# Performance work log

Measured on AMD Instinct MI355X. Metric: run time of the kernel, lower is better.

The kernel has to match this reference:

```python
import jax, jax.numpy as jnp
import numpy as np


def setup_inputs() -> dict:
    key = jax.random.key(0)
    ks = jax.random.split(key, 24)
    N, C, D_IN, HID, EMB = 8192, 4096, 32, 128, 128
    s = 0.05
    inp = {
        "cand_feat": jax.random.normal(ks[0], (1, C, D_IN), jnp.float32),
        "graph_pos": jax.random.uniform(ks[1], (N, 3), jnp.float32),
        "graph_rad": jax.random.uniform(ks[2], (N,), jnp.float32) + 0.01,
        "L": jnp.ones((1,), jnp.float32),
        "adj": jax.random.uniform(ks[3], (N, N), jnp.float32),
        "mask": jax.random.randint(ks[4], (1, C), 0, 2, jnp.int32),
        # candidate encoder: 32 -> 128 -> 128
        "cW1": jax.random.normal(ks[5], (D_IN, 128), jnp.float32) * s,
        "cb1": jnp.zeros((128,), jnp.float32),
        "cW2": jax.random.normal(ks[6], (128, EMB), jnp.float32) * s,
        "cb2": jnp.zeros((EMB,), jnp.float32),
        # graph encoder input proj: 4 -> 128
        "gW0": jax.random.normal(ks[7], (4, HID), jnp.float32) * s,
        "gb0": jnp.zeros((HID,), jnp.float32),
        # 3 GNN layers: concat(2*HID) -> HID
        "gnnW": jax.random.normal(ks[8], (3, 2 * HID, HID), jnp.float32) * s,
        "gnnb": jnp.zeros((3, HID), jnp.float32),
        # output proj: 2*HID -> EMB
        "goW": jax.random.normal(ks[9], (2 * HID, EMB), jnp.float32) * s,
        "gob": jnp.zeros((EMB,), jnp.float32),
        # fusion: 2*EMB -> 256 -> 128 -> 1
        "fW1": jax.random.normal(ks[10], (2 * EMB, 256), jnp.float32) * s,
        "fb1": jnp.zeros((256,), jnp.float32),
        "fW2": jax.random.normal(ks[11], (256, 128), jnp.float32) * s,
        "fb2": jnp.zeros((128,), jnp.float32),
        "fW3": jax.random.normal(ks[12], (128, 1), jnp.float32) * s,
        "fb3": jnp.zeros((1,), jnp.float32),
    }
    return inp


def reference(cand_feat, graph_pos, graph_rad, L, adj, mask,
              cW1, cb1, cW2, cb2, gW0, gb0, gnnW, gnnb, goW, gob,
              fW1, fb1, fW2, fb2, fW3, fb3):
    relu = jax.nn.relu
    # ---- candidate encoder: [1, C, 32] -> [1, C, 128]
    cand_emb = relu(relu(cand_feat @ cW1 + cb1) @ cW2 + cb2)
    # ---- graph encoder ----
    node = jnp.concatenate([graph_pos / L, (graph_rad / jnp.max(graph_rad))[:, None]], axis=1)  # [N, 4]
    h = relu(node @ gW0 + gb0)  # [N, HID]
    deg = jnp.clip(jnp.sum(adj, axis=-1, keepdims=True), 1.0)  # [N, 1]
    for i in range(gnnW.shape[0]):
        agg = (adj @ h) / deg                       # degree-normalized aggregation
        h = relu(jnp.concatenate([h, agg], axis=-1) @ gnnW[i] + gnnb[i])
    h_glob = jnp.concatenate([jnp.max(h, axis=0), jnp.mean(h, axis=0)], axis=-1)  # [2*HID]
    graph_emb = h_glob @ goW + gob  # [EMB]
    # ---- fusion decoder ----
    g_exp = jnp.broadcast_to(graph_emb[None, None, :], cand_emb.shape)
    combined = jnp.concatenate([cand_emb, g_exp], axis=-1)  # [1, C, 2*EMB]
    scores = (relu(relu(combined @ fW1 + fb1) @ fW2 + fb2) @ fW3 + fb3)[..., 0]  # [1, C]
    return jnp.where(mask == 0, -jnp.inf, scores)
```

## Files before the change

### kernel.cpp

```cpp
#include <hip/hip_runtime.h>
#include <hip/hip_bf16.h>

constexpr int NN  = 8192;
constexpr int CC  = 4096;
constexpr int HD  = 128;
constexpr int KSPLIT = 16;

typedef __attribute__((ext_vector_type(8))) short bf16x8;
typedef __attribute__((ext_vector_type(4))) short s16x4;
typedef __attribute__((ext_vector_type(4))) float f32x4;

static __device__ __forceinline__ unsigned short f2bf(float f) {
  unsigned int u = __builtin_bit_cast(unsigned int, f);
  unsigned int lsb = (u >> 16) & 1u;
  u += 0x7fffu + lsb;
  return (unsigned short)(u >> 16);
}
static __device__ __forceinline__ float bf2f(unsigned short u) {
  return __builtin_bit_cast(float, ((unsigned int)u) << 16);
}

static __device__ __forceinline__ int swz(int r, int k) {
  return r * 128 + ((((k >> 3) ^ (r & 7))) << 4) + ((k & 7) * 2);
}

#define GL16(gp, lp)                                                              \
  __builtin_amdgcn_global_load_lds(                                               \
      (const __attribute__((address_space(1))) void*)(gp),                        \
      (__attribute__((address_space(3))) void*)(lp), 16, 0, 0)

__global__ __launch_bounds__(256) void k_radmax(const float* __restrict__ rad, float* out) {
  __shared__ float red[256];
  int t = threadIdx.x;
  float m = 0.0f;
  for (int i = t; i < NN; i += 256) m = fmaxf(m, rad[i]);
  red[t] = m; __syncthreads();
  for (int s = 128; s > 0; s >>= 1) {
    if (t < s) red[t] = fmaxf(red[t], red[t + s]);
    __syncthreads();
  }
  if (t == 0) out[0] = red[0];
}

__global__ __launch_bounds__(256) void k_h0(const float* __restrict__ pos, const float* __restrict__ rad,
                                            const float* __restrict__ Lp, const float* __restrict__ rmax,
                                            const float* __restrict__ gW0, const float* __restrict__ gb0,
                                            float* __restrict__ h, unsigned short* __restrict__ hT) {
  __shared__ __align__(16) unsigned short lt[128][72];
  int t = threadIdx.x;
  int i0 = blockIdx.x * 64;
  float invL = 1.0f / Lp[0];
  float invR = 1.0f / rmax[0];
  for (int rep = 0; rep < 32; ++rep) {
    int idx = rep * 256 + t;
    int il = idx >> 7, j = idx & 127;
    int i = i0 + il;
    float n0 = pos[i * 3 + 0] * invL, n1 = pos[i * 3 + 1] * invL, n2 = pos[i * 3 + 2] * invL;
    float n3 = rad[i] * invR;
    float v = gb0[j] + n0 * gW0[j] + n1 * gW0[128 + j] + n2 * gW0[256 + j] + n3 * gW0[384 + j];
    v = fmaxf(v, 0.0f);
    h[(size_t)i * HD + j] = v;
    lt[j][il] = f2bf(v);
  }
  __syncthreads();
  int j = t >> 1, half = t & 1;
  unsigned short* dst = hT + (size_t)j * NN + i0 + half * 32;
  const uint4* src = (const uint4*)&lt[j][half * 32];
  uint4* d4 = (uint4*)dst;
  d4[0] = src[0]; d4[1] = src[1]; d4[2] = src[2]; d4[3] = src[3];
}

template <int SRC, int WRITEB, int DEG>
__global__ __launch_bounds__(256) void k_gemm(const float* __restrict__ A32,
                                              const unsigned short* __restrict__ A16,
                                              const unsigned short* __restrict__ hT,
                                              unsigned short* __restrict__ adjb,
                                              float* __restrict__ part_deg,
                                              unsigned short* __restrict__ part) {
  __shared__ uint4 AsQ[512];
  __shared__ uint4 BsQ[1024];
  char* As = (char*)AsQ;
  char* Bs = (char*)BsQ;
  const int t = threadIdx.x;
  const int bm = blockIdx.x;
  const int ks = blockIdx.y;
  const int kchunk = NN / KSPLIT;
  const int kbase = ks * kchunk;
  const int ksteps = kchunk / 64;

  const int lane = t & 63, w = t >> 6;
  const int wr = (w >> 1) * 32, wc = (w & 1) * 64;
  const int lr = lane & 15, lk4 = (lane >> 4) * 4;

  f32x4 acc[2][4];
  #pragma unroll
  for (int a = 0; a < 2; ++a)
    #pragma unroll
    for (int b = 0; b < 4; ++b) acc[a][b] = f32x4{0.f, 0.f, 0.f, 0.f};

  const int srow = t >> 3;
  const int sgl  = (t & 7) ^ (srow & 7);
  const unsigned short* bSrc[4];
  #pragma unroll
  for (int it = 0; it < 4; ++it)
    bSrc[it] = hT + (size_t)(it * 32 + srow) * NN + kbase + sgl * 8;

  const unsigned short* aSrc[2];
  if (SRC == 1) {
    #pragma unroll
    for (int it = 0; it < 2; ++it)
      aSrc[it] = A16 + (size_t)(bm * 64 + it * 32 + srow) * NN + kbase + sgl * 8;
  }
  const int ar = t >> 2, agq = (t & 3) * 2;
  const float* a32Src = nullptr;
  if (SRC == 0) a32Src = A32 + (size_t)(bm * 64 + ar) * NN + kbase + agq * 8;

  float rs = 0.f;

  for (int step = 0; step < ksteps; ++step) {
    __syncthreads();
    if (SRC == 1) {
      GL16(aSrc[0] + step * 64, As + t * 16);
      GL16(aSrc[1] + step * 64, As + 4096 + t * 16);
      #pragma unroll
      for (int it = 0; it < 4; ++it)
        GL16(bSrc[it] + step * 64, Bs + it * 4096 + t * 16);
    } else {
      const float* src = a32Src + step * 64;
      float4 v0 = ((const float4*)src)[0], v1 = ((const float4*)src)[1];
      float4 v2 = ((const float4*)src)[2], v3 = ((const float4*)src)[3];
      union { unsigned short u[16]; uint4 q[2]; } pk;
      pk.u[0]  = f2bf(v0.x); pk.u[1]  = f2bf(v0.y); pk.u[2]  = f2bf(v0.z); pk.u[3]  = f2bf(v0.w);
      pk.u[4]  = f2bf(v1.x); pk.u[5]  = f2bf(v1.y); pk.u[6]  = f2bf(v1.z); pk.u[7]  = f2bf(v1.w);
      pk.u[8]  = f2bf(v2.x); pk.u[9]  = f2bf(v2.y); pk.u[10] = f2bf(v2.z); pk.u[11] = f2bf(v2.w);
      pk.u[12] = f2bf(v3.x); pk.u[13] = f2bf(v3.y); pk.u[14] = f2bf(v3.z); pk.u[15] = f2bf(v3.w);
      if (DEG) rs += v0.x + v0.y + v0.z + v0.w + v1.x + v1.y + v1.z + v1.w
                   + v2.x + v2.y + v2.z + v2.w + v3.x + v3.y + v3.z + v3.w;
      if (WRITEB) {
        uint4* wdst = (uint4*)(adjb + (size_t)(bm * 64 + ar) * NN + kbase + step * 64 + agq * 8);
        wdst[0] = pk.q[0]; wdst[1] = pk.q[1];
      }
      *(uint4*)(As + ar * 128 + ((agq ^ (ar & 7)) << 4))       = pk.q[0];
      *(uint4*)(As + ar * 128 + (((agq + 1) ^ (ar & 7)) << 4)) = pk.q[1];
      #pragma unroll
      for (int it = 0; it < 4; ++it)
        GL16(bSrc[it] + step * 64, Bs + it * 4096 + t * 16);
    }
    __syncthreads();
    #pragma unroll
    for (int kk = 0; kk < 2; ++kk) {
      int klo = kk * 32 + lk4;
      bf16x8 a[2];
      #pragma unroll
      for (int mi = 0; mi < 2; ++mi) {
        int r = wr + mi * 16 + lr;
        union { bf16x8 v; s16x4 p[2]; } ua;
        ua.p[0] = *(const s16x4*)(As + swz(r, klo));
        ua.p[1] = *(const s16x4*)(As + swz(r, klo + 16));
        a[mi] = ua.v;
      }
      #pragma unroll
      for (int ni = 0; ni < 4; ++ni) {
        int rn = wc + ni * 16 + lr;
        union { bf16x8 v; s16x4 p[2]; } ub;
        ub.p[0] = *(const s16x4*)(Bs + swz(rn, klo));
        ub.p[1] = *(const s16x4*)(Bs + swz(rn, klo + 16));
        bf16x8 b = ub.v;
        #pragma unroll
        for (int mi = 0; mi < 2; ++mi)
          acc[mi][ni] = __builtin_amdgcn_mfma_f32_16x16x32_bf16(a[mi], b, acc[mi][ni], 0, 0, 0);
      }
    }
  }

  if (DEG) {
    float v = rs;
    v += __shfl_xor(v, 1);
    v += __shfl_xor(v, 2);
    if ((t & 3) == 0) part_deg[(size_t)ks * NN + bm * 64 + ar] = v;
  }

  unsigned short* outb = part + (size_t)ks * NN * HD;
  #pragma unroll
  for (int mi = 0; mi < 2; ++mi) {
    int rowb = bm * 64 + wr + mi * 16 + (lane >> 4) * 4;
    #pragma unroll
    for (int ni = 0; ni < 4; ++ni) {
      int col = wc + ni * 16 + lr;
      #pragma unroll
      for (int j = 0; j < 4; ++j)
        outb[(size_t)(rowb + j) * HD + col] = f2bf(acc[mi][ni][j]);
    }
  }
}

__global__ __launch_bounds__(256) void k_update(const unsigned short* __restrict__ part,
                                                const float* __restrict__ part_deg,
                                                const float* __restrict__ hin,
                                                const float* __restrict__ W, const float* __restrict__ bias,
                                                float* __restrict__ hout, unsigned short* __restrict__ hT,
                                                int last) {
  __shared__ float cc[16][256];
  __shared__ __align__(16) unsigned short lt2[128][24];
  int t = threadIdx.x;
  int r0 = blockIdx.x * 16;
  for (int rep = 0; rep < 8; ++rep) {
    int idx = rep * 256 + t;
    int rl = idx >> 7, j = idx & 127;
    int row = r0 + rl;
    float s = 0.f, d = 0.f;
    for (int ks = 0; ks < KSPLIT; ++ks) {
      s += bf2f(part[((size_t)ks * NN + row) * HD + j]);
      d += part_deg[(size_t)ks * NN + row];
    }
    d = fmaxf(d, 1.0f);
    cc[rl][128 + j] = s / d;
    cc[rl][j] = hin[(size_t)row * HD + j];
  }
  __syncthreads();
  int jo = t & 127, rbase = t >> 7;
  float accv[8];
  float bj = bias[jo];
  for (int rr = 0; rr < 8; ++rr) accv[rr] = bj;
  for (int jj = 0; jj < 256; ++jj) {
    float wv = W[jj * HD + jo];
    for (int rr = 0; rr < 8; ++rr) accv[rr] += cc[rbase + rr * 2][jj] * wv;
  }
  for (int rr = 0; rr < 8; ++rr) {
    int rl = rbase + rr * 2;
    float v = fmaxf(accv[rr], 0.f);
    hout[(size_t)(r0 + rl) * HD + jo] = v;
    if (!last) lt2[jo][rl] = f2bf(v);
  }
  if (!last) {
    __syncthreads();
    int j = t >> 1, half = t & 1;
    *(uint4*)(hT + (size_t)j * NN + r0 + half * 8) = *(const uint4*)&lt2[j][half * 8];
  }
}

__global__ __launch_bounds__(256) void k_pool(const float* __restrict__ h,
                                              float* __restrict__ pmax, float* __restrict__ psum) {
  int b = blockIdx.x, t = threadIdx.x;
  int j = t & 127, half = t >> 7;
  int r0 = b * 128 + half * 64;
  float mx = -1e30f, sm = 0.f;
  for (int r = r0; r < r0 + 64; ++r) {
    float v = h[(size_t)r * HD + j];
    mx = fmaxf(mx, v); sm += v;
  }
  __shared__ float lm[2][128], ls[2][128];
  lm[half][j] = mx; ls[half][j] = sm;
  __syncthreads();
  if (half == 0) {
    pmax[b * 128 + j] = fmaxf(lm[0][j], lm[1][j]);
    psum[b * 128 + j] = ls[0][j] + ls[1][j];
  }
}

__global__ __launch_bounds__(256) void k_glob(const float* __restrict__ pmax, const float* __restrict__ psum,
                                              const float* __restrict__ goW, const float* __restrict__ gob,
                                              float* __restrict__ ge) {
  __shared__ float hg[256];
  int t = threadIdx.x;
  int j = t & 127, which = t >> 7;
  if (which == 0) {
    float m = -1e30f;
    for (int b = 0; b < 64; ++b) m = fmaxf(m, pmax[b * 128 + j]);
    hg[j] = m;
  } else {
    float s = 0.f;
    for (int b = 0; b < 64; ++b) s += psum[b * 128 + j];
    hg[128 + j] = s * (1.0f / (float)NN);
  }
  __syncthreads();
  if (t < 128) {
    float s = gob[t];
    for (int jj = 0; jj < 256; ++jj) s += hg[jj] * goW[jj * HD + t];
    ge[t] = s;
  }
}

__global__ __launch_bounds__(256) void k_fusion(const float* __restrict__ cand, const float* __restrict__ ge,
                                                const int* __restrict__ mask,
                                                const float* __restrict__ cW1, const float* __restrict__ cb1,
                                                const float* __restrict__ cW2, const float* __restrict__ cb2,
                                                const float* __restrict__ fW1, const float* __restrict__ fb1,
                                                const float* __restrict__ fW2, const float* __restrict__ fb2,
                                                const float* __restrict__ fW3, const float* __restrict__ fb3,
                                                float* __restrict__ out) {
  __shared__ float x[16][32];
  __shared__ float t1[16][128];
  __shared__ float t2[16][128];
  __shared__ float u1[16][256];
  __shared__ float u2[16][129];
  __shared__ float geL[128];
  int t = threadIdx.x;
  int c0 = blockIdx.x * 16;
  if (t < 128) geL[t] = ge[t];
  for (int rep = 0; rep < 2; ++rep) {
    int idx = rep * 256 + t;
    int cl = idx >> 5, d = idx & 31;
    x[cl][d] = cand[(size_t)(c0 + cl) * 32 + d];
  }
  __syncthreads();
  {
    int j = t & 127, cg = (t >> 7) * 8;
    float a[8]; float bj = cb1[j];
    for (int q = 0; q < 8; ++q) a[q] = bj;
    for (int d = 0; d < 32; ++d) {
      float wv = cW1[d * 128 + j];
      for (int q = 0; q < 8; ++q) a[q] += x[cg + q][d] * wv;
    }
    for (int q = 0; q < 8; ++q) t1[cg + q][j] = fmaxf(a[q], 0.f);
  }
  __syncthreads();
  {
    int j = t & 127, cg = (t >> 7) * 8;
    float a[8]; float bj = cb2[j];
    for (int q = 0; q < 8; ++q) a[q] = bj;
    for (int d = 0; d < 128; ++d) {
      float wv = cW2[d * 128 + j];
      for (int q = 0; q < 8; ++q) a[q] += t1[cg + q][d] * wv;
    }
    for (int q = 0; q < 8; ++q) t2[cg + q][j] = fmaxf(a[q], 0.f);
  }
  __syncthreads();
  {
    int jo = t;
    float gp = fb1[jo];
    for (int d = 0; d < 128; ++d) gp += geL[d] * fW1[(128 + d) * 256 + jo];
    float a[16];
    for (int q = 0; q < 16; ++q) a[q] = gp;
    for (int d = 0; d < 128; ++d) {
      float wv = fW1[d * 256 + jo];
      for (int q = 0; q < 16; ++q) a[q] += t2[q][d] * wv;
    }
    for (int q = 0; q < 16; ++q) u1[q][jo] = fmaxf(a[q], 0.f);
  }
  __syncthreads();
  {
    int j = t & 127, cg = (t >> 7) * 8;
    float a[8]; float bj = fb2[j];
    for (int q = 0; q < 8; ++q) a[q] = bj;
    for (int d = 0; d < 256; ++d) {
      float wv = fW2[d * 128 + j];
      for (int q = 0; q < 8; ++q) a[q] += u1[cg + q][d] * wv;
    }
    for (int q = 0; q < 8; ++q) u2[cg + q][j] = fmaxf(a[q], 0.f);
  }
  __syncthreads();
  if (t < 16) {
    int c = c0 + t;
    float s = fb3[0];
    for (int d = 0; d < 128; ++d) s += u2[t][d] * fW3[d];
    out[c] = (mask[c] == 0) ? -3.0e38f : s;
  }
}

extern "C" void kernel_launch(void* const* d_in, const int* in_sizes, int n_in,
                              void* d_out, int out_size, void* d_ws, size_t ws_size,
                              hipStream_t stream) {
  const float* cand = (const float*)d_in[0];
  const float* pos  = (const float*)d_in[1];
  const float* rad  = (const float*)d_in[2];
  const float* Lp   = (const float*)d_in[3];
  const float* adj  = (const float*)d_in[4];
  const int*   mask = (const int*)d_in[5];
  const float* cW1 = (const float*)d_in[6];
  const float* cb1 = (const float*)d_in[7];
  const float* cW2 = (const float*)d_in[8];
  const float* cb2 = (const float*)d_in[9];
  const float* gW0 = (const float*)d_in[10];
  const float* gb0 = (const float*)d_in[11];
  const float* gnnW = (const float*)d_in[12];
  const float* gnnb = (const float*)d_in[13];
  const float* goW = (const float*)d_in[14];
  const float* gob = (const float*)d_in[15];
  const float* fW1 = (const float*)d_in[16];
  const float* fb1 = (const float*)d_in[17];
  const float* fW2 = (const float*)d_in[18];
  const float* fb2 = (const float*)d_in[19];
  const float* fW3 = (const float*)d_in[20];
  const float* fb3 = (const float*)d_in[21];

  char* ws = (char*)d_ws;
  float* h           = (float*)ws;
  unsigned short* hT = (unsigned short*)(ws + (4ull << 20));
  float* rmax        = (float*)(ws + (6ull << 20));
  float* pmax        = (float*)(ws + (6ull << 20) + 4096);
  float* psum        = pmax + 64 * 128;
  float* ge          = psum + 64 * 128;
  unsigned short* part = (unsigned short*)(ws + (8ull << 20));
  float* part_deg    = (float*)(ws + (40ull << 20));
  unsigned short* adjb = (unsigned short*)(ws + (41ull << 20));

  bool big = ws_size >= (41ull << 20) + (size_t)NN * NN * 2;

  k_radmax<<<1, 256, 0, stream>>>(rad, rmax);
  k_h0<<<NN / 64, 256, 0, stream>>>(pos, rad, Lp, rmax, gW0, gb0, h, hT);

  dim3 g(NN / 64, KSPLIT);
  for (int l = 0; l < 3; ++l) {
    if (l == 0) {
      if (big) k_gemm<0, 1, 1><<<g, 256, 0, stream>>>(adj, nullptr, hT, adjb, part_deg, part);
      else     k_gemm<0, 0, 1><<<g, 256, 0, stream>>>(adj, nullptr, hT, nullptr, part_deg, part);
    } else {
      if (big) k_gemm<1, 0, 0><<<g, 256, 0, stream>>>(nullptr, adjb, hT, nullptr, nullptr, part);
      else     k_gemm<0, 0, 0><<<g, 256, 0, stream>>>(adj, nullptr, hT, nullptr, nullptr, part);
    }
    k_update<<<NN / 16, 256, 0, stream>>>(part, part_deg, h,
                                          gnnW + l * 256 * HD, gnnb + l * HD, h, hT, l == 2);
  }
  k_pool<<<64, 256, 0, stream>>>(h, pmax, psum);
  k_glob<<<1, 256, 0, stream>>>(pmax, psum, goW, gob, ge);
  k_fusion<<<CC / 16, 256, 0, stream>>>(cand, ge, mask, cW1, cb1, cW2, cb2,
                                        fW1, fb1, fW2, fb2, fW3, fb3, (float*)d_out);
}
```

Measured before the change: 403.4 us.

## Split adj conversion into standalone kernel and double-buffer bf16 GEMM loads

```diff
diff --git a/kernel.cpp b/kernel.cpp
--- a/kernel.cpp
+++ b/kernel.cpp
@@ -4,7 +4,8 @@
 constexpr int NN  = 8192;
 constexpr int CC  = 4096;
 constexpr int HD  = 128;
-constexpr int KSPLIT = 16;
+constexpr int KSPLIT = 8;
+constexpr int KSTEPS = (NN / KSPLIT) / 64;
 
 typedef __attribute__((ext_vector_type(8))) short bf16x8;
 typedef __attribute__((ext_vector_type(4))) short s16x4;
@@ -70,23 +71,70 @@
   d4[0] = src[0]; d4[1] = src[1]; d4[2] = src[2]; d4[3] = src[3];
 }
 
-template <int SRC, int WRITEB, int DEG>
+template <int CONVERT>
+__global__ __launch_bounds__(256) void k_conv(const float* __restrict__ adj,
+                                              unsigned short* __restrict__ adjb,
+                                              float* __restrict__ deg) {
+  int row = blockIdx.x;
+  int t = threadIdx.x;
+  const float4* src = (const float4*)(adj + (size_t)row * NN);
+  float s = 0.f;
+  #pragma unroll
+  for (int it = 0; it < 4; ++it) {
+    int g = (it * 256 + t) * 2;
+    float4 v0 = src[g], v1 = src[g + 1];
+    s += v0.x + v0.y + v0.z + v0.w + v1.x + v1.y + v1.z + v1.w;
+    if (CONVERT) {
+      union { unsigned short u[8]; uint4 q; } pk;
+      pk.u[0] = f2bf(v0.x); pk.u[1] = f2bf(v0.y); pk.u[2] = f2bf(v0.z); pk.u[3] = f2bf(v0.w);
+      pk.u[4] = f2bf(v1.x); pk.u[5] = f2bf(v1.y); pk.u[6] = f2bf(v1.z); pk.u[7] = f2bf(v1.w);
+      *(uint4*)(adjb + (size_t)row * NN + (size_t)g * 4) = pk.q;
+    }
+  }
+  for (int o = 32; o > 0; o >>= 1) s += __shfl_down(s, o);
+  __shared__ float red[4];
+  if ((t & 63) == 0) red[t >> 6] = s;
+  __syncthreads();
+  if (t == 0) deg[row] = fmaxf(red[0] + red[1] + red[2] + red[3], 1.0f);
+}
+
+#define COMPUTE(Ab, Bb)                                                              \
+  _Pragma("unroll")                                                                  \
+  for (int kk = 0; kk < 2; ++kk) {                                                   \
+    int klo = kk * 32 + lk4;                                                         \
+    bf16x8 afr[2];                                                                   \
+    _Pragma("unroll")                                                                \
+    for (int mi = 0; mi < 2; ++mi) {                                                 \
+      int r = wr + mi * 16 + lr;                                                     \
+      union { bf16x8 v; s16x4 p[2]; } ua;                                            \
+      ua.p[0] = *(const s16x4*)((Ab) + swz(r, klo));                                 \
+      ua.p[1] = *(const s16x4*)((Ab) + swz(r, klo + 16));                            \
+      afr[mi] = ua.v;                                                                \
+    }                                                                                \
+    _Pragma("unroll")                                                                \
+    for (int ni = 0; ni < 4; ++ni) {                                                 \
+      int rn = wc + ni * 16 + lr;                                                    \
+      union { bf16x8 v; s16x4 p[2]; } ub;                                            \
+      ub.p[0] = *(const s16x4*)((Bb) + swz(rn, klo));                                \
+      ub.p[1] = *(const s16x4*)((Bb) + swz(rn, klo + 16));                           \
+      _Pragma("unroll")                                                              \
+      for (int mi = 0; mi < 2; ++mi)                                                 \
+        acc[mi][ni] = __builtin_amdgcn_mfma_f32_16x16x32_bf16(afr[mi], ub.v,         \
+                                                              acc[mi][ni], 0, 0, 0); \
+    }                                                                                \
+  }
+
+template <int SRC>
 __global__ __launch_bounds__(256) void k_gemm(const float* __restrict__ A32,
                                               const unsigned short* __restrict__ A16,
                                               const unsigned short* __restrict__ hT,
-                                              unsigned short* __restrict__ adjb,
-                                              float* __restrict__ part_deg,
                                               unsigned short* __restrict__ part) {
-  __shared__ uint4 AsQ[512];
-  __shared__ uint4 BsQ[1024];
-  char* As = (char*)AsQ;
-  char* Bs = (char*)BsQ;
+  __shared__ __align__(16) char As[2][8192];
+  __shared__ __align__(16) char Bs[2][16384];
   const int t = threadIdx.x;
   const int bm = blockIdx.x;
   const int ks = blockIdx.y;
-  const int kchunk = NN / KSPLIT;
-  const int kbase = ks * kchunk;
-  const int ksteps = kchunk / 64;
+  const int kbase = ks * (NN / KSPLIT);
 
   const int lane = t & 63, w = t >> 6;
   const int wr = (w >> 1) * 32, wc = (w & 1) * 64;
@@ -105,27 +153,43 @@
   for (int it = 0; it < 4; ++it)
     bSrc[it] = hT + (size_t)(it * 32 + srow) * NN + kbase + sgl * 8;
 
-  const unsigned short* aSrc[2];
   if (SRC == 1) {
+    const unsigned short* aSrc[2];
     #pragma unroll
     for (int it = 0; it < 2; ++it)
       aSrc[it] = A16 + (size_t)(bm * 64 + it * 32 + srow) * NN + kbase + sgl * 8;
-  }
-  const int ar = t >> 2, agq = (t & 3) * 2;
-  const float* a32Src = nullptr;
-  if (SRC == 0) a32Src = A32 + (size_t)(bm * 64 + ar) * NN + kbase + agq * 8;
-
-  float rs = 0.f;
-
-  for (int step = 0; step < ksteps; ++step) {
-    __syncthreads();
-    if (SRC == 1) {
-      GL16(aSrc[0] + step * 64, As + t * 16);
-      GL16(aSrc[1] + step * 64, As + 4096 + t * 16);
-      #pragma unroll
-      for (int it = 0; it < 4; ++it)
-        GL16(bSrc[it] + step * 64, Bs + it * 4096 + t * 16);
-    } else {
+
+#define STG(s, d) do {                                  \
+    GL16(aSrc[0] + (s) * 64, &As[d][t * 16]);           \
+    GL16(aSrc[1] + (s) * 64, &As[d][4096 + t * 16]);    \
+    GL16(bSrc[0] + (s) * 64, &Bs[d][t * 16]);           \
+    GL16(bSrc[1] + (s) * 64, &Bs[d][4096 + t * 16]);    \
+    GL16(bSrc[2] + (s) * 64, &Bs[d][8192 + t * 16]);    \
+    GL16(bSrc[3] + (s) * 64, &Bs[d][12288 + t * 16]);   \
+  } while (0)
+
+    STG(0, 0);
+    int cur = 0;
+    for (int step = 0; step < KSTEPS; ++step) {
+      if (step + 1 < KSTEPS) {
+        STG(step + 1, cur ^ 1);
+        asm volatile("s_waitcnt vmcnt(6)" ::: "memory");
+      } else {
+        asm volatile("s_waitcnt vmcnt(0)" ::: "memory");
+      }
+      __builtin_amdgcn_s_barrier();
+      __builtin_amdgcn_sched_barrier(0);
+      COMPUTE(As[cur], Bs[cur]);
+      __builtin_amdgcn_sched_barrier(0);
+      __builtin_amdgcn_s_barrier();
+      cur ^= 1;
+    }
+#undef STG
+  } else {
+    const int ar = t >> 2, agq = (t & 3) * 2;
+    const float* a32Src = A32 + (size_t)(bm * 64 + ar) * NN + kbase + agq * 8;
+    for (int step = 0; step < KSTEPS; ++step) {
+      __syncthreads();
       const float* src = a32Src + step * 64;
       float4 v0 = ((const float4*)src)[0], v1 = ((const float4*)src)[1];
       float4 v2 = ((const float4*)src)[2], v3 = ((const float4*)src)[3];
@@ -134,50 +198,14 @@
       pk.u[4]  = f2bf(v1.x); pk.u[5]  = f2bf(v1.y); pk.u[6]  = f2bf(v1.z); pk.u[7]  = f2bf(v1.w);
       pk.u[8]  = f2bf(v2.x); pk.u[9]  = f2bf(v2.y); pk.u[10] = f2bf(v2.z); pk.u[11] = f2bf(v2.w);
       pk.u[12] = f2bf(v3.x); pk.u[13] = f2bf(v3.y); pk.u[14] = f2bf(v3.z); pk.u[15] = f2bf(v3.w);
-      if (DEG) rs += v0.x + v0.y + v0.z + v0.w + v1.x + v1.y + v1.z + v1.w
-                   + v2.x + v2.y + v2.z + v2.w + v3.x + v3.y + v3.z + v3.w;
-      if (WRITEB) {
-        uint4* wdst = (uint4*)(adjb + (size_t)(bm * 64 + ar) * NN + kbase + step * 64 + agq * 8);
-        wdst[0] = pk.q[0]; wdst[1] = pk.q[1];
-      }
-      *(uint4*)(As + ar * 128 + ((agq ^ (ar & 7)) << 4))       = pk.q[0];
-      *(uint4*)(As + ar * 128 + (((agq + 1) ^ (ar & 7)) << 4)) = pk.q[1];
+      *(uint4*)(&As[0][ar * 128 + ((agq ^ (ar & 7)) << 4)])       = pk.q[0];
+      *(uint4*)(&As[0][ar * 128 + (((agq + 1) ^ (ar & 7)) << 4)]) = pk.q[1];
       #pragma unroll
       for (int it = 0; it < 4; ++it)
-        GL16(bSrc[it] + step * 64, Bs + it * 4096 + t * 16);
-    }
-    __syncthreads();
-    #pragma unroll
-    for (int kk = 0; kk < 2; ++kk) {
-      int klo = kk * 32 + lk4;
-      bf16x8 a[2];
-      #pragma unroll
-      for (int mi = 0; mi < 2; ++mi) {
-        int r = wr + mi * 16 + lr;
-        union { bf16x8 v; s16x4 p[2]; } ua;
-        ua.p[0] = *(const s16x4*)(As + swz(r, klo));
-        ua.p[1] = *(const s16x4*)(As + swz(r, klo + 16));
-        a[mi] = ua.v;
-      }
-      #pragma unroll
-      for (int ni = 0; ni < 4; ++ni) {
-        int rn = wc + ni * 16 + lr;
-        union { bf16x8 v; s16x4 p[2]; } ub;
-        ub.p[0] = *(const s16x4*)(Bs + swz(rn, klo));
-        ub.p[1] = *(const s16x4*)(Bs + swz(rn, klo + 16));
-        bf16x8 b = ub.v;
-        #pragma unroll
-        for (int mi = 0; mi < 2; ++mi)
-          acc[mi][ni] = __builtin_amdgcn_mfma_f32_16x16x32_bf16(a[mi], b, acc[mi][ni], 0, 0, 0);
-      }
-    }
-  }
-
-  if (DEG) {
-    float v = rs;
-    v += __shfl_xor(v, 1);
-    v += __shfl_xor(v, 2);
-    if ((t & 3) == 0) part_deg[(size_t)ks * NN + bm * 64 + ar] = v;
+        GL16(bSrc[it] + step * 64, &Bs[0][it * 4096 + t * 16]);
+      __syncthreads();
+      COMPUTE(As[0], Bs[0]);
+    }
   }
 
   unsigned short* outb = part + (size_t)ks * NN * HD;
@@ -195,7 +223,7 @@
 }
 
 __global__ __launch_bounds__(256) void k_update(const unsigned short* __restrict__ part,
-                                                const float* __restrict__ part_deg,
+                                                const float* __restrict__ deg,
                                                 const float* __restrict__ hin,
                                                 const float* __restrict__ W, const float* __restrict__ bias,
                                                 float* __restrict__ hout, unsigned short* __restrict__ hT,
@@ -208,13 +236,10 @@
     int idx = rep * 256 + t;
     int rl = idx >> 7, j = idx & 127;
     int row = r0 + rl;
-    float s = 0.f, d = 0.f;
-    for (int ks = 0; ks < KSPLIT; ++ks) {
+    float s = 0.f;
+    for (int ks = 0; ks < KSPLIT; ++ks)
       s += bf2f(part[((size_t)ks * NN + row) * HD + j]);
-      d += part_deg[(size_t)ks * NN + row];
-    }
-    d = fmaxf(d, 1.0f);
-    cc[rl][128 + j] = s / d;
+    cc[rl][128 + j] = s / deg[row];
     cc[rl][j] = hin[(size_t)row * HD + j];
   }
   __syncthreads();
@@ -391,25 +416,22 @@
   float* pmax        = (float*)(ws + (6ull << 20) + 4096);
   float* psum        = pmax + 64 * 128;
   float* ge          = psum + 64 * 128;
+  float* deg         = (float*)(ws + (7ull << 20));
   unsigned short* part = (unsigned short*)(ws + (8ull << 20));
-  float* part_deg    = (float*)(ws + (40ull << 20));
-  unsigned short* adjb = (unsigned short*)(ws + (41ull << 20));
-
-  bool big = ws_size >= (41ull << 20) + (size_t)NN * NN * 2;
+  unsigned short* adjb = (unsigned short*)(ws + (24ull << 20));
+
+  bool big = ws_size >= (24ull << 20) + (size_t)NN * NN * 2;
 
   k_radmax<<<1, 256, 0, stream>>>(rad, rmax);
   k_h0<<<NN / 64, 256, 0, stream>>>(pos, rad, Lp, rmax, gW0, gb0, h, hT);
+  if (big) k_conv<1><<<NN, 256, 0, stream>>>(adj, adjb, deg);
+  else     k_conv<0><<<NN, 256, 0, stream>>>(adj, nullptr, deg);
 
   dim3 g(NN / 64, KSPLIT);
   for (int l = 0; l < 3; ++l) {
-    if (l == 0) {
-      if (big) k_gemm<0, 1, 1><<<g, 256, 0, stream>>>(adj, nullptr, hT, adjb, part_deg, part);
-      else     k_gemm<0, 0, 1><<<g, 256, 0, stream>>>(adj, nullptr, hT, nullptr, part_deg, part);
-    } else {
-      if (big) k_gemm<1, 0, 0><<<g, 256, 0, stream>>>(nullptr, adjb, hT, nullptr, nullptr, part);
-      else     k_gemm<0, 0, 0><<<g, 256, 0, stream>>>(adj, nullptr, hT, nullptr, nullptr, part);
-    }
-    k_update<<<NN / 16, 256, 0, stream>>>(part, part_deg, h,
+    if (big) k_gemm<1><<<g, 256, 0, stream>>>(nullptr, adjb, hT, part);
+    else     k_gemm<0><<<g, 256, 0, stream>>>(adj, nullptr, hT, part);
+    k_update<<<NN / 16, 256, 0, stream>>>(part, deg, h,
                                           gnnW + l * 256 * HD, gnnb + l * HD, h, hT, l == 2);
   }
   k_pool<<<64, 256, 0, stream>>>(h, pmax, psum);
```

After: 421.2 us. +4.4%, slower.

## Replace LDS-tiled aggregation GEMM with direct-to-register MFMA loads and halve K-split

Applied to the files above, without the earlier changes.

```diff
diff --git a/kernel.cpp b/kernel.cpp
--- a/kernel.cpp
+++ b/kernel.cpp
@@ -4,7 +4,9 @@
 constexpr int NN  = 8192;
 constexpr int CC  = 4096;
 constexpr int HD  = 128;
-constexpr int KSPLIT = 16;
+constexpr int KSPLIT = 8;
+constexpr int KCHUNK = NN / KSPLIT;
+constexpr int KSTEPS = KCHUNK / 32;
 
 typedef __attribute__((ext_vector_type(8))) short bf16x8;
 typedef __attribute__((ext_vector_type(4))) short s16x4;
@@ -19,15 +21,6 @@
 static __device__ __forceinline__ float bf2f(unsigned short u) {
   return __builtin_bit_cast(float, ((unsigned int)u) << 16);
 }
-
-static __device__ __forceinline__ int swz(int r, int k) {
-  return r * 128 + ((((k >> 3) ^ (r & 7))) << 4) + ((k & 7) * 2);
-}
-
-#define GL16(gp, lp)                                                              \
-  __builtin_amdgcn_global_load_lds(                                               \
-      (const __attribute__((address_space(1))) void*)(gp),                        \
-      (__attribute__((address_space(3))) void*)(lp), 16, 0, 0)
 
 __global__ __launch_bounds__(256) void k_radmax(const float* __restrict__ rad, float* out) {
   __shared__ float red[256];
@@ -70,127 +63,80 @@
   d4[0] = src[0]; d4[1] = src[1]; d4[2] = src[2]; d4[3] = src[3];
 }
 
-template <int SRC, int WRITEB, int DEG>
+template <int SRC, int WB, int DG>
 __global__ __launch_bounds__(256) void k_gemm(const float* __restrict__ A32,
                                               const unsigned short* __restrict__ A16,
                                               const unsigned short* __restrict__ hT,
                                               unsigned short* __restrict__ adjb,
                                               float* __restrict__ part_deg,
                                               unsigned short* __restrict__ part) {
-  __shared__ uint4 AsQ[512];
-  __shared__ uint4 BsQ[1024];
-  char* As = (char*)AsQ;
-  char* Bs = (char*)BsQ;
   const int t = threadIdx.x;
   const int bm = blockIdx.x;
   const int ks = blockIdx.y;
-  const int kchunk = NN / KSPLIT;
-  const int kbase = ks * kchunk;
-  const int ksteps = kchunk / 64;
-
+  const int kbase = ks * KCHUNK;
   const int lane = t & 63, w = t >> 6;
-  const int wr = (w >> 1) * 32, wc = (w & 1) * 64;
-  const int lr = lane & 15, lk4 = (lane >> 4) * 4;
-
-  f32x4 acc[2][4];
+  const int rb = bm * 64 + w * 16;
+  const int lr = lane & 15, kg = lane >> 4;
+  const int klo = kg * 4;
+  const int arow = rb + lr;
+
+  f32x4 acc[8];
   #pragma unroll
-  for (int a = 0; a < 2; ++a)
+  for (int ni = 0; ni < 8; ++ni) acc[ni] = f32x4{0.f, 0.f, 0.f, 0.f};
+
+  const unsigned short* bp[8];
+  #pragma unroll
+  for (int ni = 0; ni < 8; ++ni)
+    bp[ni] = hT + (size_t)(ni * 16 + lr) * NN + kbase + klo;
+
+  const unsigned short* ap16 = nullptr;
+  const float* ap32 = nullptr;
+  if (SRC == 1) ap16 = A16 + (size_t)arow * NN + kbase + klo;
+  else          ap32 = A32 + (size_t)arow * NN + kbase + klo;
+
+  float rs = 0.f;
+
+  for (int step = 0; step < KSTEPS; ++step) {
+    const int k0 = step * 32;
+    union { bf16x8 v; s16x4 p[2]; } ua;
+    if (SRC == 1) {
+      ua.p[0] = *(const s16x4*)(ap16 + k0);
+      ua.p[1] = *(const s16x4*)(ap16 + k0 + 16);
+    } else {
+      float4 v0 = *(const float4*)(ap32 + k0);
+      float4 v1 = *(const float4*)(ap32 + k0 + 16);
+      union { unsigned short u[4]; s16x4 s; ushort4 q; } lo, hi;
+      lo.u[0] = f2bf(v0.x); lo.u[1] = f2bf(v0.y); lo.u[2] = f2bf(v0.z); lo.u[3] = f2bf(v0.w);
+      hi.u[0] = f2bf(v1.x); hi.u[1] = f2bf(v1.y); hi.u[2] = f2bf(v1.z); hi.u[3] = f2bf(v1.w);
+      ua.p[0] = lo.s; ua.p[1] = hi.s;
+      if (DG) rs += v0.x + v0.y + v0.z + v0.w + v1.x + v1.y + v1.z + v1.w;
+      if (WB) {
+        unsigned short* wb = adjb + (size_t)arow * NN + kbase + k0 + klo;
+        *(ushort4*)wb = lo.q;
+        *(ushort4*)(wb + 16) = hi.q;
+      }
+    }
     #pragma unroll
-    for (int b = 0; b < 4; ++b) acc[a][b] = f32x4{0.f, 0.f, 0.f, 0.f};
-
-  const int srow = t >> 3;
-  const int sgl  = (t & 7) ^ (srow & 7);
-  const unsigned short* bSrc[4];
-  #pragma unroll
-  for (int it = 0; it < 4; ++it)
-    bSrc[it] = hT + (size_t)(it * 32 + srow) * NN + kbase + sgl * 8;
-
-  const unsigned short* aSrc[2];
-  if (SRC == 1) {
-    #pragma unroll
-    for (int it = 0; it < 2; ++it)
-      aSrc[it] = A16 + (size_t)(bm * 64 + it * 32 + srow) * NN + kbase + sgl * 8;
-  }
-  const int ar = t >> 2, agq = (t & 3) * 2;
-  const float* a32Src = nullptr;
-  if (SRC == 0) a32Src = A32 + (size_t)(bm * 64 + ar) * NN + kbase + agq * 8;
-
-  float rs = 0.f;
-
-  for (int step = 0; step < ksteps; ++step) {
-    __syncthreads();
-    if (SRC == 1) {
-      GL16(aSrc[0] + step * 64, As + t * 16);
-      GL16(aSrc[1] + step * 64, As + 4096 + t * 16);
-      #pragma unroll
-      for (int it = 0; it < 4; ++it)
-        GL16(bSrc[it] + step * 64, Bs + it * 4096 + t * 16);
-    } else {
-      const float* src = a32Src + step * 64;
-      float4 v0 = ((const float4*)src)[0], v1 = ((const float4*)src)[1];
-      float4 v2 = ((const float4*)src)[2], v3 = ((const float4*)src)[3];
-      union { unsigned short u[16]; uint4 q[2]; } pk;
-      pk.u[0]  = f2bf(v0.x); pk.u[1]  = f2bf(v0.y); pk.u[2]  = f2bf(v0.z); pk.u[3]  = f2bf(v0.w);
-      pk.u[4]  = f2bf(v1.x); pk.u[5]  = f2bf(v1.y); pk.u[6]  = f2bf(v1.z); pk.u[7]  = f2bf(v1.w);
-      pk.u[8]  = f2bf(v2.x); pk.u[9]  = f2bf(v2.y); pk.u[10] = f2bf(v2.z); pk.u[11] = f2bf(v2.w);
-      pk.u[12] = f2bf(v3.x); pk.u[13] = f2bf(v3.y); pk.u[14] = f2bf(v3.z); pk.u[15] = f2bf(v3.w);
-      if (DEG) rs += v0.x + v0.y + v0.z + v0.w + v1.x + v1.y + v1.z + v1.w
-                   + v2.x + v2.y + v2.z + v2.w + v3.x + v3.y + v3.z + v3.w;
-      if (WRITEB) {
-        uint4* wdst = (uint4*)(adjb + (size_t)(bm * 64 + ar) * NN + kbase + step * 64 + agq * 8);
-        wdst[0] = pk.q[0]; wdst[1] = pk.q[1];
-      }
-      *(uint4*)(As + ar * 128 + ((agq ^ (ar & 7)) << 4))       = pk.q[0];
-      *(uint4*)(As + ar * 128 + (((agq + 1) ^ (ar & 7)) << 4)) = pk.q[1];
-      #pragma unroll
-      for (int it = 0; it < 4; ++it)
-        GL16(bSrc[it] + step * 64, Bs + it * 4096 + t * 16);
-    }
-    __syncthreads();
-    #pragma unroll
-    for (int kk = 0; kk < 2; ++kk) {
-      int klo = kk * 32 + lk4;
-      bf16x8 a[2];
-      #pragma unroll
-      for (int mi = 0; mi < 2; ++mi) {
-        int r = wr + mi * 16 + lr;
-        union { bf16x8 v; s16x4 p[2]; } ua;
-        ua.p[0] = *(const s16x4*)(As + swz(r, klo));
-        ua.p[1] = *(const s16x4*)(As + swz(r, klo + 16));
-        a[mi] = ua.v;
-      }
-      #pragma unroll
-      for (int ni = 0; ni < 4; ++ni) {
-        int rn = wc + ni * 16 + lr;
-        union { bf16x8 v; s16x4 p[2]; } ub;
-        ub.p[0] = *(const s16x4*)(Bs + swz(rn, klo));
-        ub.p[1] = *(const s16x4*)(Bs + swz(rn, klo + 16));
-        bf16x8 b = ub.v;
-        #pragma unroll
-        for (int mi = 0; mi < 2; ++mi)
-          acc[mi][ni] = __builtin_amdgcn_mfma_f32_16x16x32_bf16(a[mi], b, acc[mi][ni], 0, 0, 0);
-      }
-    }
-  }
-
-  if (DEG) {
-    float v = rs;
-    v += __shfl_xor(v, 1);
-    v += __shfl_xor(v, 2);
-    if ((t & 3) == 0) part_deg[(size_t)ks * NN + bm * 64 + ar] = v;
+    for (int ni = 0; ni < 8; ++ni) {
+      union { bf16x8 v; s16x4 p[2]; } ub;
+      ub.p[0] = *(const s16x4*)(bp[ni] + k0);
+      ub.p[1] = *(const s16x4*)(bp[ni] + k0 + 16);
+      acc[ni] = __builtin_amdgcn_mfma_f32_16x16x32_bf16(ua.v, ub.v, acc[ni], 0, 0, 0);
+    }
+  }
+
+  if (DG) {
+    rs += __shfl_xor(rs, 16);
+    rs += __shfl_xor(rs, 32);
+    if (lane < 16) part_deg[(size_t)ks * NN + rb + lane] = rs;
   }
 
   unsigned short* outb = part + (size_t)ks * NN * HD;
   #pragma unroll
-  for (int mi = 0; mi < 2; ++mi) {
-    int rowb = bm * 64 + wr + mi * 16 + (lane >> 4) * 4;
+  for (int ni = 0; ni < 8; ++ni) {
     #pragma unroll
-    for (int ni = 0; ni < 4; ++ni) {
-      int col = wc + ni * 16 + lr;
-      #pragma unroll
-      for (int j = 0; j < 4; ++j)
-        outb[(size_t)(rowb + j) * HD + col] = f2bf(acc[mi][ni][j]);
-    }
+    for (int j = 0; j < 4; ++j)
+      outb[(size_t)(rb + kg * 4 + j) * HD + ni * 16 + lr] = f2bf(acc[ni][j]);
   }
 }
 
@@ -201,20 +147,24 @@
                                                 float* __restrict__ hout, unsigned short* __restrict__ hT,
                                                 int last) {
   __shared__ float cc[16][256];
+  __shared__ float degS[16];
   __shared__ __align__(16) unsigned short lt2[128][24];
   int t = threadIdx.x;
   int r0 = blockIdx.x * 16;
+  if (t < 16) {
+    float d = 0.f;
+    for (int ks = 0; ks < KSPLIT; ++ks) d += part_deg[(size_t)ks * NN + r0 + t];
+    degS[t] = fmaxf(d, 1.0f);
+  }
+  __syncthreads();
   for (int rep = 0; rep < 8; ++rep) {
     int idx = rep * 256 + t;
     int rl = idx >> 7, j = idx & 127;
     int row = r0 + rl;
-    float s = 0.f, d = 0.f;
-    for (int ks = 0; ks < KSPLIT; ++ks) {
+    float s = 0.f;
+    for (int ks = 0; ks < KSPLIT; ++ks)
       s += bf2f(part[((size_t)ks * NN + row) * HD + j]);
-      d += part_deg[(size_t)ks * NN + row];
-    }
-    d = fmaxf(d, 1.0f);
-    cc[rl][128 + j] = s / d;
+    cc[rl][128 + j] = s / degS[rl];
     cc[rl][j] = hin[(size_t)row * HD + j];
   }
   __syncthreads();
@@ -391,11 +341,11 @@
   float* pmax        = (float*)(ws + (6ull << 20) + 4096);
   float* psum        = pmax + 64 * 128;
   float* ge          = psum + 64 * 128;
+  float* part_deg    = (float*)(ws + (7ull << 20));
   unsigned short* part = (unsigned short*)(ws + (8ull << 20));
-  float* part_deg    = (float*)(ws + (40ull << 20));
-  unsigned short* adjb = (unsigned short*)(ws + (41ull << 20));
-
-  bool big = ws_size >= (41ull << 20) + (size_t)NN * NN * 2;
+  unsigned short* adjb = (unsigned short*)(ws + (24ull << 20));
+
+  bool big = ws_size >= (24ull << 20) + (size_t)NN * NN * 2;
 
   k_radmax<<<1, 256, 0, stream>>>(rad, rmax);
   k_h0<<<NN / 64, 256, 0, stream>>>(pos, rad, Lp, rmax, gW0, gb0, h, hT);
```

After: 1.017 ms. 2.52x slower.
